# Kernel tuning notes

Hardware: AMD Instinct MI355X
Metric: run time of the kernel (lower is better)

The kernel has to match this reference:

```python
import jax, jax.numpy as jnp
import numpy as np

B, S, D, H = 2, 2048, 1024, 16
HD = D // H  # head depth


def setup_inputs() -> dict:
    key = jax.random.key(0)
    ks = jax.random.split(key, 8)
    scale = 0.02
    K = jax.random.normal(ks[0], (B, S, D), jnp.float32)
    V = jax.random.normal(ks[1], (B, S, D), jnp.float32)
    Q = jax.random.normal(ks[2], (B, S, D), jnp.float32)
    # causal additive mask: 1.0 where attention is disallowed (strict upper triangle)
    mask = jnp.broadcast_to(
        jnp.triu(jnp.ones((S, S), jnp.float32), k=1)[None, None, :, :], (B, 1, S, S)
    )
    Wk = jax.random.normal(ks[3], (D, D), jnp.float32) * scale
    Wv = jax.random.normal(ks[4], (D, D), jnp.float32) * scale
    Wq = jax.random.normal(ks[5], (D, D), jnp.float32) * scale
    Wo = jax.random.normal(ks[6], (D, D), jnp.float32) * scale
    z = jnp.zeros((D,), jnp.float32)
    return {"K": K, "V": V, "Q": Q, "mask": mask,
            "Wk": Wk, "bk": z, "Wv": Wv, "bv": z,
            "Wq": Wq, "bq": z, "Wo": Wo, "bo": z}


def _split_heads(x):  # [B,S,D] -> [B,H,S,HD]
    return x.reshape(B, S, H, HD).transpose(0, 2, 1, 3)


def reference(K, V, Q, mask, Wk, bk, Wv, bv, Wq, bq, Wo, bo):
    k = _split_heads(K @ Wk + bk)
    v = _split_heads(V @ Wv + bv)
    q = _split_heads(Q @ Wq + bq)
    # NOTE: source scales by sqrt(d_model), not sqrt(head_depth)
    logits = jnp.einsum("bhqd,bhkd->bhqk", q, k) / jnp.sqrt(jnp.float32(D))
    logits = logits + mask * (-1e9)
    attn = jax.nn.softmax(logits, axis=-1)
    out = jnp.einsum("bhqk,bhkd->bhqd", attn, v)  # [B,H,S,HD]
    out = out.transpose(0, 2, 1, 3).reshape(B, S, D)
    return out @ Wo + bo
```

## Files before the change

### kernel.cpp

```cpp
#include <hip/hip_runtime.h>
#include <hip/hip_bf16.h>

typedef unsigned short u16;
typedef unsigned int u32;
typedef unsigned long long u64;
typedef __attribute__((ext_vector_type(8))) __bf16 bf16x8;
typedef __attribute__((ext_vector_type(4))) float f32x4;

#define SEQ 2048
#define DM 1024
#define NH 16
#define HDim 64

__device__ __forceinline__ float bf_lo(u32 u) { return __uint_as_float(u << 16); }
__device__ __forceinline__ float bf_hi(u32 u) { return __uint_as_float(u & 0xffff0000u); }
__device__ __forceinline__ u16 f2bf(float f) {
    u32 u = __float_as_uint(f);
    u32 r = (u + 0x7fffu + ((u >> 16) & 1u)) >> 16;
    return (u16)r;
}
__device__ __forceinline__ float bf2f(u16 h) { return __uint_as_float(((u32)h) << 16); }

#define GLD16(g, l)                                                         \
    __builtin_amdgcn_global_load_lds(                                       \
        (const __attribute__((address_space(1))) void*)(g),                 \
        (__attribute__((address_space(3))) void*)(l), 16, 0, 0)

__device__ __forceinline__ bool detect_f32(const u32* q)
{
    const u32 w = q[threadIdx.x & 63];
    const int e0 = ((w & 0xffffu) >> 7) & 0xff;
    const int e1 = (w >> 23) & 0xff;
    const unsigned long long b = __ballot(e0 >= 0x90 || e1 >= 0x90);
    return b != 0ull;
}

__global__ __launch_bounds__(256)
void prep_all(const void* __restrict__ Qin, const void* __restrict__ Kin,
              const void* __restrict__ Vin,
              const void* __restrict__ w0, const void* __restrict__ w1,
              const void* __restrict__ w2, const void* __restrict__ w3,
              const void* __restrict__ b0, const void* __restrict__ b1,
              const void* __restrict__ b2, const void* __restrict__ b3,
              u16* __restrict__ Xall, u16* __restrict__ Wtall,
              u16* __restrict__ ball)
{
    __shared__ u16 T[64 * 66];
    const bool f = detect_f32((const u32*)Qin);
    const int t = threadIdx.x;
    const int bid = blockIdx.x;

    if (bid < 6144) {
        const int z = bid >> 11;
        const int bx = bid & 2047;
        const void* src = (z == 0) ? Qin : (z == 1) ? Kin : Vin;
        const size_t i0 = ((size_t)bx * 256 + t) * 8;
        u16* d = Xall + (size_t)z * 4194304 + i0;
        if (f) {
            const uint4* s = reinterpret_cast<const uint4*>((const float*)src + i0);
            uint4 a = s[0], b = s[1];
            u16 o[8];
            o[0] = f2bf(__uint_as_float(a.x)); o[1] = f2bf(__uint_as_float(a.y));
            o[2] = f2bf(__uint_as_float(a.z)); o[3] = f2bf(__uint_as_float(a.w));
            o[4] = f2bf(__uint_as_float(b.x)); o[5] = f2bf(__uint_as_float(b.y));
            o[6] = f2bf(__uint_as_float(b.z)); o[7] = f2bf(__uint_as_float(b.w));
            *reinterpret_cast<uint4*>(d) = *reinterpret_cast<const uint4*>(o);
        } else {
            *reinterpret_cast<uint4*>(d) =
                *reinterpret_cast<const uint4*>((const u16*)src + i0);
        }
    } else if (bid < 7168) {
        const int r = bid - 6144;
        const int z = r >> 8;
        const void* src = (z == 0) ? w0 : (z == 1) ? w1 : (z == 2) ? w2 : w3;
        const int n0 = ((r >> 4) & 15) * 64;
        const int k0 = (r & 15) * 64;
        const int c = t & 63, g = t >> 6;
        if (f) {
            const float* W = (const float*)src;
#pragma unroll
            for (int i = 0; i < 16; i++) {
                const int kl = g * 16 + i;
                T[kl * 66 + c] = f2bf(W[(size_t)(k0 + kl) * DM + n0 + c]);
            }
        } else {
            const u16* W = (const u16*)src;
#pragma unroll
            for (int i = 0; i < 16; i++) {
                const int kl = g * 16 + i;
                T[kl * 66 + c] = W[(size_t)(k0 + kl) * DM + n0 + c];
            }
        }
        __syncthreads();
        u16* dst = Wtall + (size_t)z * 1048576;
#pragma unroll
        for (int i = 0; i < 16; i++) {
            const int nl = g * 16 + i;
            dst[(size_t)(n0 + nl) * DM + k0 + c] = T[c * 66 + nl];
        }
    } else {
#pragma unroll
        for (int j = 0; j < 16; j++) {
            const int idx = t * 16 + j;
            const int z = idx >> 10, e = idx & 1023;
            const void* src = (z == 0) ? b0 : (z == 1) ? b1 : (z == 2) ? b2 : b3;
            ball[idx] = f ? f2bf(((const float*)src)[e]) : ((const u16*)src)[e];
        }
    }
}

__global__ __launch_bounds__(256)
void gemm128(const u16* __restrict__ Xall, const u16* __restrict__ Wtall,
             const u16* __restrict__ ball, u16* __restrict__ Yall)
{
    __shared__ __align__(16) u16 As[2][128 * 32];
    __shared__ __align__(16) u16 Bs[2][128 * 32];

    const int zz = blockIdx.z;
    const bool swp = (zz != 2);
    const u16* X  = Xall + (size_t)zz * 4194304;
    const u16* Wt = Wtall + (size_t)zz * 1048576;

    const int t    = threadIdx.x;
    const int w    = t >> 6;
    const int lane = t & 63;
    const int quad = lane >> 4;
    const int ln   = lane & 15;
    const int m0   = blockIdx.y * 128;
    const int n0   = blockIdx.x * 128;

    f32x4 acc[4][4];
#pragma unroll
    for (int i = 0; i < 4; i++)
#pragma unroll
        for (int j = 0; j < 4; j++) acc[i][j] = (f32x4){0.f, 0.f, 0.f, 0.f};

    const int swz = (lane >> 3) & 3;
    const u16* ag = X  + (size_t)(m0 + w * 32 + (lane >> 2)) * DM + ((lane & 3) ^ swz) * 8;
    const u16* bg = Wt + (size_t)(n0 + w * 32 + (lane >> 2)) * DM + ((lane & 3) ^ swz) * 8;

    const int wr = (w >> 1) * 64;
    const int wc = (w & 1) * 64;
    const int rs = (quad ^ ((ln >> 1) & 3)) * 8;

#define GSTAGE(B)                                        \
    {                                                    \
        GLD16(ag,           &As[B][w * 1024]);           \
        GLD16(ag + 16 * DM, &As[B][w * 1024 + 512]);     \
        GLD16(bg,           &Bs[B][w * 1024]);           \
        GLD16(bg + 16 * DM, &Bs[B][w * 1024 + 512]);     \
        ag += 32; bg += 32;                              \
    }

#define GCOMP(B)                                                              \
    {                                                                         \
        bf16x8 af[4], bfr[4];                                                 \
        _Pragma("unroll") for (int rt = 0; rt < 4; rt++)                      \
            af[rt] = *reinterpret_cast<const bf16x8*>(                        \
                &As[B][(wr + rt * 16 + ln) * 32 + rs]);                       \
        _Pragma("unroll") for (int ct = 0; ct < 4; ct++)                      \
            bfr[ct] = *reinterpret_cast<const bf16x8*>(                       \
                &Bs[B][(wc + ct * 16 + ln) * 32 + rs]);                       \
        if (swp) {                                                            \
            _Pragma("unroll") for (int rt = 0; rt < 4; rt++)                  \
                _Pragma("unroll") for (int ct = 0; ct < 4; ct++)              \
                    acc[rt][ct] = __builtin_amdgcn_mfma_f32_16x16x32_bf16(    \
                        bfr[ct], af[rt], acc[rt][ct], 0, 0, 0);               \
        } else {                                                              \
            _Pragma("unroll") for (int rt = 0; rt < 4; rt++)                  \
                _Pragma("unroll") for (int ct = 0; ct < 4; ct++)              \
                    acc[rt][ct] = __builtin_amdgcn_mfma_f32_16x16x32_bf16(    \
                        af[rt], bfr[ct], acc[rt][ct], 0, 0, 0);               \
        }                                                                     \
    }

    GSTAGE(0);
    __syncthreads();
#pragma unroll 1
    for (int it = 0; it < 15; ++it) {
        GSTAGE(1); GCOMP(0); __syncthreads();
        GSTAGE(0); GCOMP(1); __syncthreads();
    }
    GSTAGE(1); GCOMP(0); __syncthreads();
    GCOMP(1);
#undef GSTAGE
#undef GCOMP

    u16* Y = Yall + (size_t)zz * 4194304;

    if (swp) {
        const float scale = (zz == 0) ? 0.03125f : 1.0f;
#pragma unroll
        for (int ct = 0; ct < 4; ct++) {
            const int nb = n0 + wc + ct * 16 + quad * 4;
            const int h = nb >> 6, hd = nb & (HDim - 1);
            float bv[4];
#pragma unroll
            for (int r = 0; r < 4; r++) bv[r] = bf2f(ball[zz * 1024 + nb + r]);
#pragma unroll
            for (int rt = 0; rt < 4; rt++) {
                const int m = m0 + wr + rt * 16 + ln;
                const int b = m >> 11, s = m & (SEQ - 1);
                u16 o4[4];
#pragma unroll
                for (int r = 0; r < 4; r++)
                    o4[r] = f2bf((acc[rt][ct][r] + bv[r]) * scale);
                *reinterpret_cast<u64*>(
                    Y + (((size_t)(b * NH + h)) * SEQ + s) * HDim + hd) =
                    *reinterpret_cast<const u64*>(o4);
            }
        }
    } else {
#pragma unroll
        for (int ct = 0; ct < 4; ct++) {
            const int n = n0 + wc + ct * 16 + ln;
            const float bv = bf2f(ball[zz * 1024 + n]);
            const int h = n >> 6, hd = n & (HDim - 1);
#pragma unroll
            for (int rt = 0; rt < 4; rt++) {
                const int m = m0 + wr + rt * 16 + quad * 4;
                const int b = m >> 11, s = m & (SEQ - 1);
                u16 o4[4];
#pragma unroll
                for (int r = 0; r < 4; r++) o4[r] = f2bf(acc[rt][ct][r] + bv);
                *reinterpret_cast<u64*>(
                    Y + (((size_t)(b * NH + h) * HDim + hd) * SEQ + s)) =
                    *reinterpret_cast<const u64*>(o4);
            }
        }
    }
}

__device__ __forceinline__ void attn_tile2(
    const u16* __restrict__ Ks, const u16* __restrict__ Vs,
    u16* __restrict__ Ps, const bf16x8& qf0, const bf16x8& qf1,
    int kt, int qrow, int w, int quad, int ln, f32x4* o, float& l)
{
    f32x4 s[4];
#pragma unroll
    for (int ct = 0; ct < 4; ct++) {
        const u16* kr = &Ks[(ct * 16 + ln) * 72 + quad * 8];
        bf16x8 kf0 = *reinterpret_cast<const bf16x8*>(kr);
        bf16x8 kf1 = *reinterpret_cast<const bf16x8*>(kr + 32);
        f32x4 z = (f32x4){0.f, 0.f, 0.f, 0.f};
        z = __builtin_amdgcn_mfma_f32_16x16x32_bf16(kf0, qf0, z, 0, 0, 0);
        s[ct] = __builtin_amdgcn_mfma_f32_16x16x32_bf16(kf1, qf1, z, 0, 0, 0);
    }
#pragma unroll
    for (int ct = 0; ct < 4; ct++) {
        u16 o4[4];
#pragma unroll
        for (int r = 0; r < 4; r++) {
            const int kcol = kt * 64 + ct * 16 + quad * 4 + r;
            const float e = (kcol <= qrow) ? __expf(s[ct][r]) : 0.f;
            l += e;
            o4[r] = f2bf(e);
        }
        *reinterpret_cast<u64*>(&Ps[(w * 16 + ln) * 72 + ct * 16 + quad * 4]) =
            *reinterpret_cast<const u64*>(o4);
    }
#pragma unroll
    for (int ks = 0; ks < 2; ks++) {
        bf16x8 pf = *reinterpret_cast<const bf16x8*>(
            &Ps[(w * 16 + ln) * 72 + ks * 32 + quad * 8]);
#pragma unroll
        for (int nt = 0; nt < 4; nt++) {
            bf16x8 vf = *reinterpret_cast<const bf16x8*>(
                &Vs[(nt * 16 + ln) * 72 + ks * 32 + quad * 8]);
            o[nt] = __builtin_amdgcn_mfma_f32_16x16x32_bf16(pf, vf, o[nt], 0, 0, 0);
        }
    }
}

__global__ __launch_bounds__(256)
void attn_split(const u16* __restrict__ qh, const u16* __restrict__ kh,
                const u16* __restrict__ vt, u16* __restrict__ Opart,
                float* __restrict__ Lpart)
{
    __shared__ __align__(16) u16 Ks[64 * 72];
    __shared__ __align__(16) u16 Vs[64 * 72];
    __shared__ __align__(16) u16 Ps[64 * 72];

    const int t    = threadIdx.x;
    const int i    = blockIdx.x;
    const int bh   = blockIdx.y;
    const int c    = blockIdx.z;
    const int w    = t >> 6;
    const int lane = t & 63;
    const int quad = lane >> 4;
    const int ln   = lane & 15;
    const int qtH  = 31 - i;
    const int qtL  = i;
    const int m    = (i >= 8) ? 8 : 16 - i;
    const int kt0  = c ? m : 0;
    const int kt1  = c ? (qtH + 1) : m;

    const size_t kbase = (size_t)bh * SEQ * HDim;
    const size_t vbase = (size_t)bh * HDim * SEQ;

    const u16* qrH = qh + kbase + (size_t)(qtH * 64 + w * 16 + ln) * HDim;
    const bf16x8 qfH0 = *reinterpret_cast<const bf16x8*>(qrH + quad * 8);
    const bf16x8 qfH1 = *reinterpret_cast<const bf16x8*>(qrH + 32 + quad * 8);
    const u16* qrL = qh + kbase + (size_t)(qtL * 64 + w * 16 + ln) * HDim;
    const bf16x8 qfL0 = *reinterpret_cast<const bf16x8*>(qrL + quad * 8);
    const bf16x8 qfL1 = *reinterpret_cast<const bf16x8*>(qrL + 32 + quad * 8);

    f32x4 oH[4], oL[4];
    float lH = 0.f, lL = 0.f;
#pragma unroll
    for (int k = 0; k < 4; k++) {
        oH[k] = (f32x4){0.f, 0.f, 0.f, 0.f};
        oL[k] = (f32x4){0.f, 0.f, 0.f, 0.f};
    }

    const int srow = t >> 2;
    const int sc   = (t & 3) * 16;
    const int rowH = qtH * 64 + w * 16 + ln;
    const int rowL = qtL * 64 + w * 16 + ln;

    uint4 kr0, kr1, vr0, vr1;
    {
        const uint4* ksp = reinterpret_cast<const uint4*>(
            kh + kbase + (size_t)(kt0 * 64 + srow) * HDim + sc);
        kr0 = ksp[0]; kr1 = ksp[1];
        const uint4* vsp = reinterpret_cast<const uint4*>(
            vt + vbase + (size_t)srow * SEQ + kt0 * 64 + sc);
        vr0 = vsp[0]; vr1 = vsp[1];
    }

    for (int kt = kt0; kt < kt1; kt++) {
        {
            uint4* kd = reinterpret_cast<uint4*>(&Ks[srow * 72 + sc]);
            kd[0] = kr0; kd[1] = kr1;
            uint4* vd = reinterpret_cast<uint4*>(&Vs[srow * 72 + sc]);
            vd[0] = vr0; vd[1] = vr1;
        }
        __syncthreads();

        if (kt + 1 < kt1) {
            const uint4* ksp = reinterpret_cast<const uint4*>(
                kh + kbase + (size_t)((kt + 1) * 64 + srow) * HDim + sc);
            kr0 = ksp[0]; kr1 = ksp[1];
            const uint4* vsp = reinterpret_cast<const uint4*>(
                vt + vbase + (size_t)srow * SEQ + (kt + 1) * 64 + sc);
            vr0 = vsp[0]; vr1 = vsp[1];
            __builtin_amdgcn_sched_barrier(0);
        }

        attn_tile2(Ks, Vs, Ps, qfH0, qfH1, kt, rowH, w, quad, ln, oH, lH);
        if (kt <= qtL)
            attn_tile2(Ks, Vs, Ps, qfL0, qfL1, kt, rowL, w, quad, ln, oL, lL);

        __syncthreads();
    }

    lH += __shfl_xor(lH, 16); lH += __shfl_xor(lH, 32);
    lL += __shfl_xor(lL, 16); lL += __shfl_xor(lL, 32);

    const size_t cb = ((size_t)c * 32 + bh) * SEQ;
    if (lane < 16) {
        Lpart[cb + qtH * 64 + w * 16 + lane] = lH;
        Lpart[cb + qtL * 64 + w * 16 + lane] = lL;
    }
#pragma unroll
    for (int r = 0; r < 4; r++) {
        const int rH = qtH * 64 + w * 16 + quad * 4 + r;
        const int rL = qtL * 64 + w * 16 + quad * 4 + r;
        u16* dH = Opart + (cb + rH) * HDim + ln;
        u16* dL = Opart + (cb + rL) * HDim + ln;
#pragma unroll
        for (int nt = 0; nt < 4; nt++) {
            dH[nt * 16] = f2bf(oH[nt][r]);
            dL[nt * 16] = f2bf(oL[nt][r]);
        }
    }
}

__global__ __launch_bounds__(256)
void attn_merge(const u16* __restrict__ Opart, const float* __restrict__ Lpart,
                u16* __restrict__ ctx)
{
    const size_t tid8 = (size_t)blockIdx.x * 256 + threadIdx.x;
    const int d8 = (int)(tid8 & 7);
    const int s  = (int)((tid8 >> 3) & (SEQ - 1));
    const int bh = (int)(tid8 >> 14);
    const size_t CSTR = (size_t)32 * SEQ * HDim;

    const uint4 a = *reinterpret_cast<const uint4*>(Opart + tid8 * 8);
    const uint4 b = *reinterpret_cast<const uint4*>(Opart + CSTR + tid8 * 8);
    const float l0 = Lpart[(size_t)bh * SEQ + s];
    const float l1 = Lpart[(size_t)32 * SEQ + (size_t)bh * SEQ + s];
    const float inv = 1.f / (l0 + l1);

    const u32 aw[4] = {a.x, a.y, a.z, a.w};
    const u32 bw[4] = {b.x, b.y, b.z, b.w};
    u32 ow[4];
#pragma unroll
    for (int p = 0; p < 4; p++) {
        const float lo = (bf_lo(aw[p]) + bf_lo(bw[p])) * inv;
        const float hi = (bf_hi(aw[p]) + bf_hi(bw[p])) * inv;
        ow[p] = (u32)f2bf(lo) | ((u32)f2bf(hi) << 16);
    }
    const int bb = bh >> 4, h = bh & 15;
    *reinterpret_cast<uint4*>(
        ctx + ((size_t)(bb * SEQ + s)) * DM + h * HDim + d8 * 8) =
        *reinterpret_cast<const uint4*>(ow);
}

__global__ __launch_bounds__(256)
void gemm_out(const u16* __restrict__ ctx, const u16* __restrict__ Wt,
              const u16* __restrict__ bias, void* __restrict__ dout,
              const u32* __restrict__ qdet)
{
    __shared__ __align__(16) u16 As[2][128 * 32];
    __shared__ __align__(16) u16 Bs[2][64 * 32];

    const int t    = threadIdx.x;
    const int w    = t >> 6;
    const int lane = t & 63;
    const int quad = lane >> 4;
    const int ln   = lane & 15;
    const int m0   = blockIdx.y * 128;
    const int n0   = blockIdx.x * 64;

    f32x4 acc[4][2];
#pragma unroll
    for (int i = 0; i < 4; i++)
#pragma unroll
        for (int j = 0; j < 2; j++) acc[i][j] = (f32x4){0.f, 0.f, 0.f, 0.f};

    const int swz = (lane >> 3) & 3;
    const u16* ag = ctx + (size_t)(m0 + w * 32 + (lane >> 2)) * DM + ((lane & 3) ^ swz) * 8;
    const u16* bg = Wt + (size_t)(n0 + w * 16 + (lane >> 2)) * DM + ((lane & 3) ^ swz) * 8;

    const int wr = (w >> 1) * 64;
    const int wc = (w & 1) * 32;
    const int rs = (quad ^ ((ln >> 1) & 3)) * 8;

#define OSTAGE(B)                                        \
    {                                                    \
        GLD16(ag,           &As[B][w * 1024]);           \
        GLD16(ag + 16 * DM, &As[B][w * 1024 + 512]);     \
        GLD16(bg,           &Bs[B][w * 512]);            \
        ag += 32; bg += 32;                              \
    }

#define OCOMP(B)                                                              \
    {                                                                         \
        bf16x8 af[4], bfr[2];                                                 \
        _Pragma("unroll") for (int rt = 0; rt < 4; rt++)                      \
            af[rt] = *reinterpret_cast<const bf16x8*>(                        \
                &As[B][(wr + rt * 16 + ln) * 32 + rs]);                       \
        _Pragma("unroll") for (int ct = 0; ct < 2; ct++)                      \
            bfr[ct] = *reinterpret_cast<const bf16x8*>(                       \
                &Bs[B][(wc + ct * 16 + ln) * 32 + rs]);                       \
        _Pragma("unroll") for (int rt = 0; rt < 4; rt++)                      \
            _Pragma("unroll") for (int ct = 0; ct < 2; ct++)                  \
                acc[rt][ct] = __builtin_amdgcn_mfma_f32_16x16x32_bf16(        \
                    af[rt], bfr[ct], acc[rt][ct], 0, 0, 0);                   \
    }

    OSTAGE(0);
    __syncthreads();
#pragma unroll 1
    for (int it = 0; it < 15; ++it) {
        OSTAGE(1); OCOMP(0); __syncthreads();
        OSTAGE(0); OCOMP(1); __syncthreads();
    }
    OSTAGE(1); OCOMP(0); __syncthreads();
    OCOMP(1);
#undef OSTAGE
#undef OCOMP

    const bool f = detect_f32(qdet);
#pragma unroll
    for (int ct = 0; ct < 2; ct++) {
        const int n = n0 + wc + ct * 16 + ln;
        const float bv = bf2f(bias[n]);
#pragma unroll
        for (int rt = 0; rt < 4; rt++) {
            const int mb = m0 + wr + rt * 16 + quad * 4;
#pragma unroll
            for (int r = 0; r < 4; r++) {
                const float val = acc[rt][ct][r] + bv;
                if (f) ((float*)dout)[(size_t)(mb + r) * DM + n] = val;
                else   ((u16*)dout)[(size_t)(mb + r) * DM + n] = f2bf(val);
            }
        }
    }
}

__global__ __launch_bounds__(64)
void detect_dtype(const u32* __restrict__ q, int* __restrict__ flag)
{
    const int t = threadIdx.x;
    const u32 w = q[t];
    const int e0 = ((w & 0xffffu) >> 7) & 0xff;
    const int e1 = (w >> 23) & 0xff;
    const unsigned long long b = __ballot(e0 >= 0x90 || e1 >= 0x90);
    if (t == 0) *flag = (b != 0ull) ? 1 : 0;
}

struct AttnAcc { f32x4 o[4]; float l[4]; };

__device__ __forceinline__ void attn_tile(
    const u16* __restrict__ Ks, const u16* __restrict__ Vs,
    u16* __restrict__ Ps, const bf16x8& qf0, const bf16x8& qf1,
    int kt, int rowb, int w, int quad, int ln, AttnAcc& a)
{
    f32x4 s[4];
#pragma unroll
    for (int ct = 0; ct < 4; ct++) {
        const u16* kr = &Ks[(ct * 16 + ln) * 72 + quad * 8];
        bf16x8 kf0 = *reinterpret_cast<const bf16x8*>(kr);
        bf16x8 kf1 = *reinterpret_cast<const bf16x8*>(kr + 32);
        f32x4 z = (f32x4){0.f, 0.f, 0.f, 0.f};
        z = __builtin_amdgcn_mfma_f32_16x16x32_bf16(qf0, kf0, z, 0, 0, 0);
        s[ct] = __builtin_amdgcn_mfma_f32_16x16x32_bf16(qf1, kf1, z, 0, 0, 0);
    }
#pragma unroll
    for (int ct = 0; ct < 4; ct++) {
        const int kcol = kt * 64 + ct * 16 + ln;
#pragma unroll
        for (int r = 0; r < 4; r++) {
            const float e = (kcol <= rowb + r) ? __expf(s[ct][r]) : 0.f;
            a.l[r] += e;
            Ps[(w * 16 + quad * 4 + r) * 68 + ct * 16 + ln] = f2bf(e);
        }
    }
#pragma unroll
    for (int ks = 0; ks < 2; ks++) {
        bf16x8 pf = *reinterpret_cast<const bf16x8*>(
            &Ps[(w * 16 + ln) * 68 + ks * 32 + quad * 8]);
#pragma unroll
        for (int nt = 0; nt < 4; nt++) {
            bf16x8 vf = *reinterpret_cast<const bf16x8*>(
                &Vs[(nt * 16 + ln) * 72 + ks * 32 + quad * 8]);
            a.o[nt] = __builtin_amdgcn_mfma_f32_16x16x32_bf16(pf, vf, a.o[nt], 0, 0, 0);
        }
    }
}

__global__ __launch_bounds__(256)
void attn_mfma(const u16* __restrict__ qh, const u16* __restrict__ kh,
               const u16* __restrict__ vt, u16* __restrict__ ctx)
{
    __shared__ __align__(16) u16 Ks[64 * 72];
    __shared__ __align__(16) u16 Vs[64 * 72];
    __shared__ __align__(16) u16 Ps[64 * 68];

    const int t    = threadIdx.x;
    const int i    = blockIdx.x;
    const int bh   = blockIdx.y;
    const int w    = t >> 6;
    const int lane = t & 63;
    const int quad = lane >> 4;
    const int ln   = lane & 15;
    const int qtH  = 31 - i;
    const int qtL  = i;

    const size_t kbase = (size_t)bh * SEQ * HDim;
    const size_t vbase = (size_t)bh * HDim * SEQ;

    const u16* qrH = qh + kbase + (size_t)(qtH * 64 + w * 16 + ln) * HDim;
    const bf16x8 qfH0 = *reinterpret_cast<const bf16x8*>(qrH + quad * 8);
    const bf16x8 qfH1 = *reinterpret_cast<const bf16x8*>(qrH + 32 + quad * 8);
    const u16* qrL = qh + kbase + (size_t)(qtL * 64 + w * 16 + ln) * HDim;
    const bf16x8 qfL0 = *reinterpret_cast<const bf16x8*>(qrL + quad * 8);
    const bf16x8 qfL1 = *reinterpret_cast<const bf16x8*>(qrL + 32 + quad * 8);

    AttnAcc aH, aL;
#pragma unroll
    for (int k = 0; k < 4; k++) {
        aH.o[k] = (f32x4){0.f, 0.f, 0.f, 0.f}; aH.l[k] = 0.f;
        aL.o[k] = (f32x4){0.f, 0.f, 0.f, 0.f}; aL.l[k] = 0.f;
    }

    const int srow = t >> 2;
    const int sc   = (t & 3) * 16;
    const int rowHb = qtH * 64 + w * 16 + quad * 4;
    const int rowLb = qtL * 64 + w * 16 + quad * 4;

    for (int kt = 0; kt <= qtH; kt++) {
        {
            const uint4* ks = reinterpret_cast<const uint4*>(
                kh + kbase + (size_t)(kt * 64 + srow) * HDim + sc);
            uint4* kd = reinterpret_cast<uint4*>(&Ks[srow * 72 + sc]);
            kd[0] = ks[0];
            kd[1] = ks[1];
            const uint4* vs = reinterpret_cast<const uint4*>(
                vt + vbase + (size_t)srow * SEQ + kt * 64 + sc);
            uint4* vd = reinterpret_cast<uint4*>(&Vs[srow * 72 + sc]);
            vd[0] = vs[0];
            vd[1] = vs[1];
        }
        __syncthreads();

        attn_tile(Ks, Vs, Ps, qfH0, qfH1, kt, rowHb, w, quad, ln, aH);
        if (kt <= qtL)
            attn_tile(Ks, Vs, Ps, qfL0, qfL1, kt, rowLb, w, quad, ln, aL);

        __syncthreads();
    }

#pragma unroll
    for (int m = 1; m < 16; m <<= 1) {
#pragma unroll
        for (int r = 0; r < 4; r++) {
            aH.l[r] += __shfl_xor(aH.l[r], m);
            aL.l[r] += __shfl_xor(aL.l[r], m);
        }
    }

    const int b = bh >> 4;
    const int h = bh & 15;
#pragma unroll
    for (int r = 0; r < 4; r++) {
        const float invH = 1.f / aH.l[r];
        const float invL = 1.f / aL.l[r];
        const int sH = qtH * 64 + w * 16 + quad * 4 + r;
        const int sL = qtL * 64 + w * 16 + quad * 4 + r;
        u16* dH = ctx + ((size_t)(b * SEQ + sH)) * DM + h * HDim + ln;
        u16* dL = ctx + ((size_t)(b * SEQ + sL)) * DM + h * HDim + ln;
#pragma unroll
        for (int nt = 0; nt < 4; nt++) {
            dH[nt * 16] = f2bf(aH.o[nt][r] * invH);
            dL[nt * 16] = f2bf(aL.o[nt][r] * invL);
        }
    }
}

__global__ __launch_bounds__(256)
void gemm_bias(const void* __restrict__ Xv, const void* __restrict__ Wv,
               const void* __restrict__ biasv, void* __restrict__ Yv,
               int M, int N, int K, int mode, int xsel, int wsel, int ysel,
               float scale, const int* __restrict__ flagp)
{
    __shared__ __align__(16) u16 As[64 * 32];
    __shared__ __align__(16) u16 Bs[64 * 40];

    const int f  = *flagp;
    const bool xf = (xsel != 0) && (f != 0);
    const bool wf = (wsel != 0) && (f != 0);
    const bool yf = (ysel != 0) && (f != 0);

    const u16*   Xb = (const u16*)Xv;
    const float* Xf = (const float*)Xv;
    const u16*   Wb = (const u16*)Wv;
    const float* Wf = (const float*)Wv;

    const int t    = threadIdx.x;
    const int m0   = blockIdx.y * 64;
    const int n0   = blockIdx.x * 64;
    const int w    = t >> 6;
    const int lane = t & 63;
    const int quad = lane >> 4;
    const int ln   = lane & 15;

    f32x4 acc[4];
#pragma unroll
    for (int i = 0; i < 4; i++) acc[i] = (f32x4){0.f, 0.f, 0.f, 0.f};

    const int a_row = t >> 2;
    const int a_c8  = (t & 3) * 8;
    const int b_n   = t & 63;
    const int b_k8  = (t >> 6) * 8;

    for (int kk = 0; kk < K; kk += 32) {
        const size_t aoff = (size_t)(m0 + a_row) * K + kk + a_c8;
        if (!xf) {
            *reinterpret_cast<uint4*>(&As[a_row * 32 + a_c8]) =
                *reinterpret_cast<const uint4*>(Xb + aoff);
        } else {
            const float* src = Xf + aoff;
            uint4 u0 = reinterpret_cast<const uint4*>(src)[0];
            uint4 u1 = reinterpret_cast<const uint4*>(src)[1];
            u16 tmp[8];
            tmp[0] = f2bf(__uint_as_float(u0.x));
            tmp[1] = f2bf(__uint_as_float(u0.y));
            tmp[2] = f2bf(__uint_as_float(u0.z));
            tmp[3] = f2bf(__uint_as_float(u0.w));
            tmp[4] = f2bf(__uint_as_float(u1.x));
            tmp[5] = f2bf(__uint_as_float(u1.y));
            tmp[6] = f2bf(__uint_as_float(u1.z));
            tmp[7] = f2bf(__uint_as_float(u1.w));
            *reinterpret_cast<uint4*>(&As[a_row * 32 + a_c8]) =
                *reinterpret_cast<const uint4*>(tmp);
        }
        u16 tmp[8];
        if (!wf) {
#pragma unroll
            for (int j = 0; j < 8; j++)
                tmp[j] = Wb[(size_t)(kk + b_k8 + j) * N + n0 + b_n];
        } else {
#pragma unroll
            for (int j = 0; j < 8; j++)
                tmp[j] = f2bf(Wf[(size_t)(kk + b_k8 + j) * N + n0 + b_n]);
        }
        *reinterpret_cast<uint4*>(&Bs[b_n * 40 + b_k8]) =
            *reinterpret_cast<const uint4*>(tmp);

        __syncthreads();

        bf16x8 bfrag = *reinterpret_cast<const bf16x8*>(&Bs[(w * 16 + ln) * 40 + quad * 8]);
#pragma unroll
        for (int rt = 0; rt < 4; rt++) {
            bf16x8 afrag = *reinterpret_cast<const bf16x8*>(&As[(rt * 16 + ln) * 32 + quad * 8]);
            acc[rt] = __builtin_amdgcn_mfma_f32_16x16x32_bf16(afrag, bfrag, acc[rt], 0, 0, 0);
        }
        __syncthreads();
    }

    const int n = n0 + w * 16 + ln;
    const float bv = wf ? ((const float*)biasv)[n] : bf2f(((const u16*)biasv)[n]);
#pragma unroll
    for (int rt = 0; rt < 4; rt++) {
        if (mode == 2) {
            const int m = m0 + rt * 16 + quad * 4;
            const int b = m >> 11;
            const int s = m & (SEQ - 1);
            const int h = n >> 6;
            const int hd = n & (HDim - 1);
            u16 o4[4];
#pragma unroll
            for (int r = 0; r < 4; r++) o4[r] = f2bf((acc[rt][r] + bv) * scale);
            *reinterpret_cast<u64*>(
                (u16*)Yv + (((size_t)(b * NH + h) * HDim + hd) * SEQ + s)) =
                *reinterpret_cast<const u64*>(o4);
        } else {
#pragma unroll
            for (int r = 0; r < 4; r++) {
                const int m = m0 + rt * 16 + quad * 4 + r;
                const float val = (acc[rt][r] + bv) * scale;
                if (mode == 0) {
                    if (yf) ((float*)Yv)[(size_t)m * N + n] = val;
                    else    ((u16*)Yv)[(size_t)m * N + n] = f2bf(val);
                } else {
                    const int b = m >> 11;
                    const int s = m & (SEQ - 1);
                    const int h = n >> 6;
                    const int hd = n & (HDim - 1);
                    ((u16*)Yv)[(((size_t)(b * NH + h)) * SEQ + s) * HDim + hd] = f2bf(val);
                }
            }
        }
    }
}

extern "C" void kernel_launch(void* const* d_in, const int* in_sizes, int n_in,
                              void* d_out, int out_size, void* d_ws, size_t ws_size,
                              hipStream_t stream)
{
    const void* Kin = d_in[0];
    const void* Vin = d_in[1];
    const void* Qin = d_in[2];
    const void* Wk = d_in[4];
    const void* bk = d_in[5];
    const void* Wv = d_in[6];
    const void* bv = d_in[7];
    const void* Wq = d_in[8];
    const void* bq = d_in[9];
    const void* Wo = d_in[10];
    const void* bo = d_in[11];

    char* ws = (char*)d_ws;
    const size_t NEED = ((size_t)29360128 + 4096) * 2 + 256;

    if (ws_size >= NEED) {
        u16* Xall  = (u16*)ws;
        u16* Yall  = (u16*)ws + 12582912;
        u16* Wtall = (u16*)ws + 25165824;
        u16* ball  = (u16*)ws + 29360128;
        u16* qhp   = Yall;
        u16* khp   = Yall + 4194304;
        u16* vtp   = Yall + 8388608;
        u16* ctx   = Xall;
        u16* Opart = Xall + 4194304;
        float* Lpart = (float*)Wtall;

        hipLaunchKernelGGL(prep_all, dim3(7169), dim3(256), 0, stream,
                           Qin, Kin, Vin, Wq, Wk, Wv, Wo, bq, bk, bv, bo,
                           Xall, Wtall, ball);

        hipLaunchKernelGGL(gemm128, dim3(8, 32, 3), dim3(256), 0, stream,
                           Xall, Wtall, ball, Yall);

        hipLaunchKernelGGL(attn_split, dim3(16, 32, 2), dim3(256), 0, stream,
                           qhp, khp, vtp, Opart, Lpart);

        hipLaunchKernelGGL(attn_merge, dim3(2048), dim3(256), 0, stream,
                           Opart, Lpart, ctx);

        hipLaunchKernelGGL(gemm_out, dim3(16, 32), dim3(256), 0, stream,
                           ctx, Wtall + (size_t)3 * 1048576, ball + 3 * 1024,
                           d_out, (const u32*)Qin);
    } else {
        const size_t SEG = (size_t)2 * SEQ * DM * sizeof(u16);
        u16* qh  = (u16*)(ws);
        u16* khd = (u16*)(ws + SEG);
        u16* vtd = (u16*)(ws + 2 * SEG);
        u16* ctx = (u16*)(ws + 3 * SEG);
        int* flag = (int*)(ws + 4 * SEG);

        hipLaunchKernelGGL(detect_dtype, dim3(1), dim3(64), 0, stream,
                           (const u32*)Qin, flag);

        const int M = 2 * SEQ;
        dim3 ggrid(DM / 64, M / 64);
        dim3 gblk(256);

        hipLaunchKernelGGL(gemm_bias, ggrid, gblk, 0, stream, Qin, Wq, bq, qh,  M, DM, DM, 1, 1, 1, 0, 0.03125f, flag);
        hipLaunchKernelGGL(gemm_bias, ggrid, gblk, 0, stream, Kin, Wk, bk, khd, M, DM, DM, 1, 1, 1, 0, 1.0f,     flag);
        hipLaunchKernelGGL(gemm_bias, ggrid, gblk, 0, stream, Vin, Wv, bv, vtd, M, DM, DM, 2, 1, 1, 0, 1.0f,     flag);

        hipLaunchKernelGGL(attn_mfma, dim3(16, 2 * NH), dim3(256), 0,
                           stream, qh, khd, vtd, ctx);

        hipLaunchKernelGGL(gemm_bias, ggrid, gblk, 0, stream, ctx, Wo, bo, d_out, M, DM, DM, 0, 0, 1, 1, 1.0f, flag);
    }
}
```

Baseline: 263.5 us.

## Triple-buffer LDS in projection GEMMs with partial vmcnt waits

Both the QKV projection GEMM and the output GEMM move from double-buffered shared memory with a full __syncthreads per stage to a three-stage ring buffer. Two stages are prefetched up front, and each iteration waits only until the oldest stage's global-to-LDS loads finish (vmcnt 4 or 3) before a barrier. This lets one extra tile of loads stay in flight while computing, hiding global memory latency. In exchange it uses more LDS per block, which may lower occupancy, and its correctness depends on the hand-written vmcnt counts matching the number of loads per stage.

```diff
diff --git a/kernel.cpp b/kernel.cpp
--- a/kernel.cpp
+++ b/kernel.cpp
@@ -113,8 +113,8 @@
 void gemm128(const u16* __restrict__ Xall, const u16* __restrict__ Wtall,
              const u16* __restrict__ ball, u16* __restrict__ Yall)
 {
-    __shared__ __align__(16) u16 As[2][128 * 32];
-    __shared__ __align__(16) u16 Bs[2][128 * 32];
+    __shared__ __align__(16) u16 As[3 * 4096];
+    __shared__ __align__(16) u16 Bs[3 * 4096];
 
     const int zz = blockIdx.z;
     const bool swp = (zz != 2);
@@ -143,24 +143,27 @@
     const int wc = (w & 1) * 64;
     const int rs = (quad ^ ((ln >> 1) & 3)) * 8;
 
-#define GSTAGE(B)                                        \
-    {                                                    \
-        GLD16(ag,           &As[B][w * 1024]);           \
-        GLD16(ag + 16 * DM, &As[B][w * 1024 + 512]);     \
-        GLD16(bg,           &Bs[B][w * 1024]);           \
-        GLD16(bg + 16 * DM, &Bs[B][w * 1024 + 512]);     \
-        ag += 32; bg += 32;                              \
-    }
-
-#define GCOMP(B)                                                              \
+#define GSTAGE(S)                                          \
+    {                                                      \
+        u16* al = &As[(S) * 4096 + w * 1024];              \
+        u16* bl = &Bs[(S) * 4096 + w * 1024];              \
+        GLD16(ag,           al);                           \
+        GLD16(ag + 16 * DM, al + 512);                     \
+        GLD16(bg,           bl);                           \
+        GLD16(bg + 16 * DM, bl + 512);                     \
+        ag += 32; bg += 32;                                \
+    }
+
+#define GCOMP(S)                                                              \
     {                                                                         \
+        const int ab = (S) * 4096;                                            \
         bf16x8 af[4], bfr[4];                                                 \
         _Pragma("unroll") for (int rt = 0; rt < 4; rt++)                      \
             af[rt] = *reinterpret_cast<const bf16x8*>(                        \
-                &As[B][(wr + rt * 16 + ln) * 32 + rs]);                       \
+                &As[ab + (wr + rt * 16 + ln) * 32 + rs]);                     \
         _Pragma("unroll") for (int ct = 0; ct < 4; ct++)                      \
             bfr[ct] = *reinterpret_cast<const bf16x8*>(                       \
-                &Bs[B][(wc + ct * 16 + ln) * 32 + rs]);                       \
+                &Bs[ab + (wc + ct * 16 + ln) * 32 + rs]);                     \
         if (swp) {                                                            \
             _Pragma("unroll") for (int rt = 0; rt < 4; rt++)                  \
                 _Pragma("unroll") for (int ct = 0; ct < 4; ct++)              \
@@ -175,14 +178,20 @@
     }
 
     GSTAGE(0);
-    __syncthreads();
+    GSTAGE(1);
+    int cs = 0, ss = 2;
 #pragma unroll 1
-    for (int it = 0; it < 15; ++it) {
-        GSTAGE(1); GCOMP(0); __syncthreads();
-        GSTAGE(0); GCOMP(1); __syncthreads();
-    }
-    GSTAGE(1); GCOMP(0); __syncthreads();
-    GCOMP(1);
+    for (int it = 0; it < 31; ++it) {
+        asm volatile("s_waitcnt vmcnt(4)" ::: "memory");
+        __builtin_amdgcn_s_barrier();
+        if (it < 30) GSTAGE(ss);
+        GCOMP(cs);
+        cs = (cs == 2) ? 0 : cs + 1;
+        ss = (ss == 2) ? 0 : ss + 1;
+    }
+    asm volatile("s_waitcnt vmcnt(0)" ::: "memory");
+    __builtin_amdgcn_s_barrier();
+    GCOMP(cs);
 #undef GSTAGE
 #undef GCOMP
 
@@ -412,8 +421,8 @@
               const u16* __restrict__ bias, void* __restrict__ dout,
               const u32* __restrict__ qdet)
 {
-    __shared__ __align__(16) u16 As[2][128 * 32];
-    __shared__ __align__(16) u16 Bs[2][64 * 32];
+    __shared__ __align__(16) u16 As[3 * 4096];
+    __shared__ __align__(16) u16 Bs[3 * 2048];
 
     const int t    = threadIdx.x;
     const int w    = t >> 6;
@@ -437,23 +446,25 @@
     const int wc = (w & 1) * 32;
     const int rs = (quad ^ ((ln >> 1) & 3)) * 8;
 
-#define OSTAGE(B)                                        \
-    {                                                    \
-        GLD16(ag,           &As[B][w * 1024]);           \
-        GLD16(ag + 16 * DM, &As[B][w * 1024 + 512]);     \
-        GLD16(bg,           &Bs[B][w * 512]);            \
-        ag += 32; bg += 32;                              \
-    }
-
-#define OCOMP(B)                                                              \
+#define OSTAGE(S)                                          \
+    {                                                      \
+        u16* al = &As[(S) * 4096 + w * 1024];              \
+        u16* bl = &Bs[(S) * 2048 + w * 512];               \
+        GLD16(ag,           al);                           \
+        GLD16(ag + 16 * DM, al + 512);                     \
+        GLD16(bg,           bl);                           \
+        ag += 32; bg += 32;                                \
+    }
+
+#define OCOMP(S)                                                              \
     {                                                                         \
         bf16x8 af[4], bfr[2];                                                 \
         _Pragma("unroll") for (int rt = 0; rt < 4; rt++)                      \
             af[rt] = *reinterpret_cast<const bf16x8*>(                        \
-                &As[B][(wr + rt * 16 + ln) * 32 + rs]);                       \
+                &As[(S) * 4096 + (wr + rt * 16 + ln) * 32 + rs]);             \
         _Pragma("unroll") for (int ct = 0; ct < 2; ct++)                      \
             bfr[ct] = *reinterpret_cast<const bf16x8*>(                       \
-                &Bs[B][(wc + ct * 16 + ln) * 32 + rs]);                       \
+                &Bs[(S) * 2048 + (wc + ct * 16 + ln) * 32 + rs]);             \
         _Pragma("unroll") for (int rt = 0; rt < 4; rt++)                      \
             _Pragma("unroll") for (int ct = 0; ct < 2; ct++)                  \
                 acc[rt][ct] = __builtin_amdgcn_mfma_f32_16x16x32_bf16(        \
@@ -461,14 +472,20 @@
     }
 
     OSTAGE(0);
-    __syncthreads();
+    OSTAGE(1);
+    int cs = 0, ss = 2;
 #pragma unroll 1
-    for (int it = 0; it < 15; ++it) {
-        OSTAGE(1); OCOMP(0); __syncthreads();
-        OSTAGE(0); OCOMP(1); __syncthreads();
-    }
-    OSTAGE(1); OCOMP(0); __syncthreads();
-    OCOMP(1);
+    for (int it = 0; it < 31; ++it) {
+        asm volatile("s_waitcnt vmcnt(3)" ::: "memory");
+        __builtin_amdgcn_s_barrier();
+        if (it < 30) OSTAGE(ss);
+        OCOMP(cs);
+        cs = (cs == 2) ? 0 : cs + 1;
+        ss = (ss == 2) ? 0 : ss + 1;
+    }
+    asm volatile("s_waitcnt vmcnt(0)" ::: "memory");
+    __builtin_amdgcn_s_barrier();
+    OCOMP(cs);
 #undef OSTAGE
 #undef OCOMP
 
```

Result: slower. 268.9 us (+2.0%).
